# Kernel tuning notes

Hardware: AMD Instinct MI355X
Metric: run time of the kernel (lower is better)

The kernel has to match this reference:

```python
import jax, jax.numpy as jnp
import numpy as np

NUM_ENT = 10000
NUM_REL = 50
HID = 64
N_TRIP = 500000


def _ramp_layer(emb_ent, emb_rel, W_res, W_me, W_mr, W_pr, h, r, t):
    num_ent, num_rel = emb_ent.shape[0], emb_rel.shape[0]
    d_out = W_me.shape[0] // num_rel
    # relation-specific projections: (num_ent, num_rel, d_out), (num_rel, num_rel, d_out)
    proj_ent = (emb_ent @ W_me.T).reshape(num_ent, num_rel, d_out)
    proj_rel = (emb_rel @ W_mr.T).reshape(num_rel, num_rel, d_out)
    diag_rel = proj_rel[jnp.arange(num_rel), jnp.arange(num_rel)]  # (num_rel, d_out)
    # gather per-triplet messages: proj_ent[h, r] + proj_rel[r, r]
    msg = proj_ent[h, r] + diag_rel[r]  # (T, d_out)
    # aggr_method == 'sum' -> div_coeff = 1
    upd = (emb_ent @ W_res.T).at[t].add(msg)  # scatter-add into tails
    return jax.nn.leaky_relu(upd, negative_slope=0.01), emb_rel @ W_pr.T


def setup_inputs() -> dict:
    key = jax.random.key(0)
    ks = jax.random.split(key, 11)
    gain = float(np.sqrt(2.0))  # relu gain

    def xavier(k, shape):
        fan_out, fan_in = shape
        std = gain * np.sqrt(2.0 / (fan_in + fan_out))
        return (jax.random.normal(k, shape, dtype=jnp.float32) * std)

    def msg_init(k, shape, d_in, d_out):
        std = gain * np.sqrt(2.0 / (d_in + d_out))
        return (jax.random.normal(k, shape, dtype=jnp.float32) * std)

    inp = {
        # layer 0: dim_in_ent=NUM_ENT, dim_in_rel=NUM_REL, dim_out=HID
        "Wres0": xavier(ks[0], (HID, NUM_ENT)),
        "Wme0": msg_init(ks[1], (NUM_REL * HID, NUM_ENT), NUM_ENT, HID),
        "Wmr0": msg_init(ks[2], (NUM_REL * HID, NUM_REL), NUM_REL, HID),
        "Wpr0": xavier(ks[3], (HID, NUM_REL)),
        # layer 1: dim_in_ent=HID, dim_in_rel=HID
        "Wres1": xavier(ks[4], (HID, HID)),
        "Wme1": msg_init(ks[5], (NUM_REL * HID, HID), HID, HID),
        "Wmr1": msg_init(ks[6], (NUM_REL * HID, HID), HID, HID),
        "Wpr1": xavier(ks[7], (HID, HID)),
        "h": jax.random.randint(ks[8], (N_TRIP,), 0, NUM_ENT),
        "r": jax.random.randint(ks[9], (N_TRIP,), 0, NUM_REL),
        "t": jax.random.randint(ks[10], (N_TRIP,), 0, NUM_ENT),
    }
    return inp


def reference(Wres0, Wme0, Wmr0, Wpr0, Wres1, Wme1, Wmr1, Wpr1, h, r, t):
    emb_ent = jnp.eye(NUM_ENT, dtype=jnp.float32)
    emb_rel = jnp.eye(NUM_REL, dtype=jnp.float32)
    emb_ent, emb_rel = _ramp_layer(emb_ent, emb_rel, Wres0, Wme0, Wmr0, Wpr0, h, r, t)
    emb_ent, emb_rel = _ramp_layer(emb_ent, emb_rel, Wres1, Wme1, Wmr1, Wpr1, h, r, t)
    return (emb_ent, emb_rel)
```

## Files before the change

### kernel.cpp

```cpp
#include <hip/hip_runtime.h>

#define NUM_ENT 10000
#define NUM_REL 50
#define HID 64
#define NTRIP 500000
#define NSLOT 51
#define SSTR (NUM_ENT * HID)
#define ETILE 128
#define NETILE 79
#define TRB (NSLOT * NETILE)
#define BSTR 192

typedef __attribute__((ext_vector_type(8))) short short8;
typedef __attribute__((ext_vector_type(4))) float f32x4;

static __device__ __forceinline__ unsigned short f2bf(float x) {
    unsigned u = __float_as_uint(x);
    return (unsigned short)((u + 0x7FFFu + ((u >> 16) & 1u)) >> 16);
}
static __device__ __forceinline__ float bf2f(unsigned short b) {
    return __uint_as_float((unsigned)b << 16);
}
static __device__ __forceinline__ short8 ld8(const unsigned short* p) {
    return *(const short8*)p;
}


__global__ __launch_bounds__(256) void k_prep(const float* __restrict__ Wmr0,
                                              const float* __restrict__ Wpr0,
                                              const float* __restrict__ Wmr1,
                                              const float* __restrict__ Wpr1,
                                              const float* __restrict__ Wme1,
                                              const float* __restrict__ Wres1,
                                              int* __restrict__ bins,
                                              float* __restrict__ diag0,
                                              float* __restrict__ diag1,
                                              float* __restrict__ outrel,
                                              unsigned short* __restrict__ Wb) {
    int bid = blockIdx.x, tid = threadIdx.x;
    if (bid < 40) {
        int i = bid * 256 + tid;
        if (i < NUM_ENT) bins[i] = 0;
        return;
    }
    bid -= 40;
    if (bid < 13) {
        int i = bid * 256 + tid;
        if (i < NSLOT * HID)
            diag0[i] = (i < NUM_REL * HID) ? Wmr0[(size_t)i * NUM_REL + (i >> 6)] : 0.f;
        return;
    }
    bid -= 13;
    if (bid < 13) {
        __shared__ float wp[4][64];
        int sub = tid >> 6, d = tid & 63;
        int rr = bid * 4 + sub;
        wp[sub][d] = (rr < NUM_REL) ? Wpr0[d * NUM_REL + rr] : 0.f;
        __syncthreads();
        if (rr < NUM_REL) {
            float s1 = 0.f, s2 = 0.f;
            const float* wmr = Wmr1 + (size_t)(rr * HID + d) * HID;
            const float* wpr = Wpr1 + d * HID;
            for (int k = 0; k < HID; k++) {
                s1 += wp[sub][k] * wmr[k];
                s2 += wp[sub][k] * wpr[k];
            }
            diag1[rr * HID + d] = s1;
            outrel[rr * HID + d] = s2;
        }
        return;
    }
    bid -= 13;
    if (bid < 816) {
        int i = bid * 256 + tid;
        if (i < NSLOT * HID * HID)
            Wb[i] = f2bf(i < NUM_REL * HID * HID ? Wme1[i]
                                                 : Wres1[i - NUM_REL * HID * HID]);
        return;
    }
    if (tid < HID) diag1[NUM_REL * HID + tid] = 0.f;
}


__global__ __launch_bounds__(256) void k_build(const float* __restrict__ Wme0,
                                               const float* __restrict__ Wres0,
                                               const float* __restrict__ diag0,
                                               unsigned short* __restrict__ P,
                                               const int* __restrict__ h,
                                               const int* __restrict__ r,
                                               const int* __restrict__ t,
                                               int* __restrict__ bins,
                                               unsigned* __restrict__ bucket2) {
    __shared__ __align__(16) unsigned utile[ETILE][32];
    __shared__ float dg[64];
    int tid = threadIdx.x;

    if (blockIdx.x >= TRB) {
        int i = ((int)blockIdx.x - TRB) * 256 + tid;
        if (i < NTRIP) {
            int tt = t[i];
            int lp = atomicAdd(&bins[tt], 1);
            if (lp < BSTR)
                bucket2[tt * BSTR + lp] =
                    (unsigned)r[i] * (unsigned)SSTR + (unsigned)h[i] * 64u;
        }
        return;
    }

    int slot = blockIdx.x / NETILE;
    int ey = blockIdx.x - slot * NETILE;
    int e0 = ey * ETILE;
    const float* Wbase = (slot < NUM_REL)
        ? Wme0 + (size_t)(slot * HID) * NUM_ENT + e0
        : Wres0 + e0;
    unsigned short* Pslot = P + (size_t)slot * SSTR;

    if (e0 + ETILE <= NUM_ENT) {
        int dp = tid >> 5;
        int kk = tid & 31;
        int x4 = kk * 4;
        int wf1 = kk & 7;
        int wf2 = kk >> 3;
        const float* p0 = Wbase + (size_t)(dp * 2 + 0) * NUM_ENT + x4;
        const float* p1 = Wbase + (size_t)(dp * 2 + 1) * NUM_ENT + x4;
        float4 vA0 = *(const float4*)(p0);
        float4 vB0 = *(const float4*)(p1);
        float4 vA1 = *(const float4*)(p0 + 16 * NUM_ENT);
        float4 vB1 = *(const float4*)(p1 + 16 * NUM_ENT);
        float4 vA2 = *(const float4*)(p0 + 32 * NUM_ENT);
        float4 vB2 = *(const float4*)(p1 + 32 * NUM_ENT);
        float4 vA3 = *(const float4*)(p0 + 48 * NUM_ENT);
        float4 vB3 = *(const float4*)(p1 + 48 * NUM_ENT);

        if (tid < 64) dg[tid] = diag0[slot * HID + tid];
        __syncthreads();

#define PACK_IT(IT, VA, VB)                                                     \
        {                                                                       \
            int d = IT * 16 + dp * 2;                                           \
            int d2 = IT * 8 + dp;                                               \
            float dgA = dg[d], dgB = dg[d + 1];                                 \
            const float* a = (const float*)&VA;                                 \
            const float* b = (const float*)&VB;                                 \
            int col = (((d2 >> 2) ^ wf1) << 2) | ((d2 & 3) ^ wf2);              \
            utile[x4 + 0][col] = (unsigned)f2bf(a[0] + dgA) |                   \
                                 ((unsigned)f2bf(b[0] + dgB) << 16);            \
            utile[x4 + 1][col] = (unsigned)f2bf(a[1] + dgA) |                   \
                                 ((unsigned)f2bf(b[1] + dgB) << 16);            \
            utile[x4 + 2][col] = (unsigned)f2bf(a[2] + dgA) |                   \
                                 ((unsigned)f2bf(b[2] + dgB) << 16);            \
            utile[x4 + 3][col] = (unsigned)f2bf(a[3] + dgA) |                   \
                                 ((unsigned)f2bf(b[3] + dgB) << 16);            \
        }
        PACK_IT(0, vA0, vB0)
        PACK_IT(1, vA1, vB1)
        PACK_IT(2, vA2, vB2)
        PACK_IT(3, vA3, vB3)
#undef PACK_IT
        __syncthreads();
#pragma unroll
        for (int it = 0; it < 4; ++it) {
            int idx = tid + it * 256;
            int ee = idx >> 3;
            int q = idx & 7;
            int f1 = (ee >> 2) & 7;
            int f2 = (ee >> 5) & 3;
            uint4 u = *(const uint4*)&utile[ee][(q ^ f1) << 2];
            unsigned ua = u.x, ub = u.y, uc = u.z, ud = u.w;
            if (f2 & 1) { unsigned s0 = ua; ua = ub; ub = s0;
                          unsigned s1 = uc; uc = ud; ud = s1; }
            if (f2 & 2) { unsigned s0 = ua; ua = uc; uc = s0;
                          unsigned s1 = ub; ub = ud; ud = s1; }
            uint4 o = make_uint4(ua, ub, uc, ud);
            *(uint4*)&Pslot[(size_t)(e0 + ee) * 64 + q * 8] = o;
        }
    } else {
        if (tid < 64) dg[tid] = diag0[slot * HID + tid];
        __syncthreads();
        int rem = NUM_ENT - e0;
        for (int i = tid; i < rem * 64; i += 256) {
            int ee = i % rem;
            int dd = i / rem;
            float v = Wbase[(size_t)dd * NUM_ENT + ee] + dg[dd];
            Pslot[(size_t)(e0 + ee) * 64 + dd] = f2bf(v);
        }
    }
}


__global__ __launch_bounds__(256) void k_gemmB(const unsigned short* __restrict__ Abf,
                                               const unsigned short* __restrict__ Wb,
                                               const float* __restrict__ diag1,
                                               unsigned short* __restrict__ B,
                                               int percut) {
    int e0 = blockIdx.x * 64;
    int rl0 = blockIdx.y * percut;
    int rl1 = rl0 + percut;
    if (rl1 > NSLOT) rl1 = NSLOT;
    int w = (int)threadIdx.x >> 6;
    int lane = (int)threadIdx.x & 63;
    int lrow = lane & 15;
    int hi = lane >> 4;
    int lk8 = hi * 8;
    int row = e0 + w * 16 + lrow;
    int rowc = row < NUM_ENT ? row : NUM_ENT - 1;
    short8 a0 = ld8(Abf + (size_t)rowc * HID + lk8);
    short8 a1 = ld8(Abf + (size_t)rowc * HID + 32 + lk8);

    for (int rl = rl0; rl < rl1; ++rl) {
        const unsigned short* wb = Wb + (size_t)rl * 4096;
        f32x4 acc[4] = {};
#pragma unroll
        for (int tt = 0; tt < 4; ++tt) {
            const unsigned short* wd = wb + (tt * 16 + lrow) * 64;
            short8 b0 = ld8(wd + lk8);
            short8 b1 = ld8(wd + 32 + lk8);
            acc[tt] = __builtin_amdgcn_mfma_f32_16x16x32_bf16(a0, b0, acc[tt], 0, 0, 0);
            acc[tt] = __builtin_amdgcn_mfma_f32_16x16x32_bf16(a1, b1, acc[tt], 0, 0, 0);
        }
        unsigned short* Bslot = B + (size_t)rl * SSTR;
#pragma unroll
        for (int tt = 0; tt < 4; ++tt) {
            float dgv = diag1[rl * HID + tt * 16 + lrow];
#pragma unroll
            for (int q = 0; q < 4; ++q) {
                int eo = e0 + w * 16 + hi * 4 + q;
                if (eo < NUM_ENT)
                    Bslot[(size_t)eo * 64 + tt * 16 + lrow] = f2bf(acc[tt][q] + dgv);
            }
        }
    }
}


__global__ __launch_bounds__(256) void k_scatter(const unsigned short* __restrict__ table,
                                                 const int* __restrict__ bins,
                                                 const unsigned* __restrict__ bucket2,
                                                 unsigned short* __restrict__ Abf,
                                                 float* __restrict__ outF,
                                                 int writeBf) {
    int e = __builtin_amdgcn_readfirstlane(blockIdx.x * 4 + (threadIdx.x >> 6));
    if (e >= NUM_ENT) return;
    int lane = threadIdx.x & 63;
    int oct = lane >> 3;
    int sl = lane & 7;
    int cnt = bins[e];
    if (cnt > BSTR) cnt = BSTR;
    int j0 = e * BSTR, j1 = j0 + cnt;
    float acc[8] = {};
    float acc2[8] = {};
    int jj = j0;
    for (; jj + 16 <= j1; jj += 16) {
        unsigned o0 = bucket2[jj + oct];
        unsigned o1 = bucket2[jj + 8 + oct];
        short8 v0 = ld8(table + o0 + sl * 8);
        short8 v1 = ld8(table + o1 + sl * 8);
#pragma unroll
        for (int k = 0; k < 8; ++k) {
            acc[k]  += bf2f(((const unsigned short*)&v0)[k]);
            acc2[k] += bf2f(((const unsigned short*)&v1)[k]);
        }
    }
    if (jj + 8 <= j1) {
        unsigned o = bucket2[jj + oct];
        short8 v = ld8(table + o + sl * 8);
#pragma unroll
        for (int k = 0; k < 8; ++k) acc[k] += bf2f(((const unsigned short*)&v)[k]);
        jj += 8;
    }
    if (oct < j1 - jj) {
        unsigned o = bucket2[jj + oct];
        short8 v = ld8(table + o + sl * 8);
#pragma unroll
        for (int k = 0; k < 8; ++k) acc2[k] += bf2f(((const unsigned short*)&v)[k]);
    }
#pragma unroll
    for (int k = 0; k < 8; ++k) {
        acc[k] += acc2[k];
        acc[k] += __shfl_xor(acc[k], 8);
        acc[k] += __shfl_xor(acc[k], 16);
        acc[k] += __shfl_xor(acc[k], 32);
    }
    if (oct == 0) {
        short8 base = ld8(table + (size_t)(NSLOT - 1) * SSTR + (size_t)e * HID + sl * 8);
        float v[8];
#pragma unroll
        for (int k = 0; k < 8; ++k) {
            float x = acc[k] + bf2f(((const unsigned short*)&base)[k]);
            v[k] = (x >= 0.f) ? x : 0.01f * x;
        }
        if (writeBf) {
            unsigned short pk[8];
#pragma unroll
            for (int k = 0; k < 8; ++k) pk[k] = f2bf(v[k]);
            *(short8*)&Abf[(size_t)e * HID + sl * 8] = *(const short8*)pk;
        } else {
            *(float4*)&outF[(size_t)e * HID + sl * 8] = make_float4(v[0], v[1], v[2], v[3]);
            *(float4*)&outF[(size_t)e * HID + sl * 8 + 4] = make_float4(v[4], v[5], v[6], v[7]);
        }
    }
}


__global__ void k_rel(const float* __restrict__ Wpr0, const float* __restrict__ Wmr1,
                      const float* __restrict__ Wpr1, float* __restrict__ diag1,
                      float* __restrict__ outrel) {
    __shared__ float wp[HID];
    int rr = blockIdx.x, d = threadIdx.x;
    wp[d] = Wpr0[d * NUM_REL + rr];
    __syncthreads();
    float s1 = 0.0f, s2 = 0.0f;
    const float* wmr = Wmr1 + (size_t)(rr * HID + d) * HID;
    const float* wpr = Wpr1 + d * HID;
    for (int k = 0; k < HID; k++) { s1 += wp[k] * wmr[k]; s2 += wp[k] * wpr[k]; }
    diag1[rr * HID + d] = s1;
    outrel[rr * HID + d] = s2;
}

__global__ void k_init_u0(const float* __restrict__ Wres0, float* __restrict__ U0) {
    __shared__ float tile[64][65];
    int e0 = blockIdx.x * 64;
    for (int i = threadIdx.x; i < 64 * 64; i += 256) {
        int dd = i >> 6, xx = i & 63;
        if (e0 + xx < NUM_ENT) tile[xx][dd] = Wres0[dd * NUM_ENT + e0 + xx];
    }
    __syncthreads();
    for (int i = threadIdx.x; i < 64 * 64; i += 256) {
        int ee = i >> 6, dd = i & 63;
        if (e0 + ee < NUM_ENT) U0[(e0 + ee) * HID + dd] = tile[ee][dd];
    }
}

__global__ void k_hist(const int* __restrict__ r, int* __restrict__ hist) {
    __shared__ int lh[NUM_REL];
    int tid = threadIdx.x;
    if (tid < NUM_REL) lh[tid] = 0;
    __syncthreads();
    int i = blockIdx.x * blockDim.x + tid;
    if (i < NTRIP) atomicAdd(&lh[r[i]], 1);
    __syncthreads();
    if (tid < NUM_REL && lh[tid] > 0) atomicAdd(&hist[tid], lh[tid]);
}

__global__ void k_scan_small(const int* __restrict__ hist, int* __restrict__ off,
                             int* __restrict__ cur) {
    if (threadIdx.x == 0 && blockIdx.x == 0) {
        int s = 0;
        for (int i = 0; i < NUM_REL; i++) { off[i] = s; cur[i] = s; s += hist[i]; }
        off[NUM_REL] = s;
    }
}

__global__ void k_bucket(const int* __restrict__ h, const int* __restrict__ r,
                         const int* __restrict__ t, int* __restrict__ cur,
                         int2* __restrict__ bucket) {
    __shared__ int lcnt[NUM_REL];
    __shared__ int lbase[NUM_REL];
    int tid = threadIdx.x;
    if (tid < NUM_REL) lcnt[tid] = 0;
    __syncthreads();
    int i = blockIdx.x * blockDim.x + tid;
    int rr = -1, lpos = 0;
    if (i < NTRIP) { rr = r[i]; lpos = atomicAdd(&lcnt[rr], 1); }
    __syncthreads();
    if (tid < NUM_REL && lcnt[tid] > 0) lbase[tid] = atomicAdd(&cur[tid], lcnt[tid]);
    __syncthreads();
    if (i < NTRIP) bucket[lbase[rr] + lpos] = make_int2(h[i], t[i]);
}

__global__ void k_l0(const float* __restrict__ Wme0, const float* __restrict__ Wmr0,
                     const int* __restrict__ off, const int2* __restrict__ bucket,
                     float* __restrict__ U0) {
    __shared__ float row[NUM_ENT];
    int rr = blockIdx.x >> 6;
    int d  = blockIdx.x & 63;
    const float4* src4 = (const float4*)(Wme0 + (size_t)(rr * HID + d) * NUM_ENT);
    float4* row4 = (float4*)row;
    for (int i = threadIdx.x; i < NUM_ENT / 4; i += blockDim.x) row4[i] = src4[i];
    __syncthreads();
    float wd0 = Wmr0[(size_t)(rr * HID + d) * NUM_REL + rr];
    int b0 = off[rr], b1 = off[rr + 1];
    for (int i = b0 + threadIdx.x; i < b1; i += blockDim.x) {
        int2 ht = bucket[i];
        atomicAdd(&U0[(size_t)ht.y * HID + d], row[ht.x] + wd0);
    }
}

__global__ void k_lrelu(float* __restrict__ x, int n) {
    int i = blockIdx.x * blockDim.x + threadIdx.x;
    if (i < n) { float v = x[i]; x[i] = v >= 0.0f ? v : 0.01f * v; }
}

__global__ void k_init_u1(const float* __restrict__ A, const float* __restrict__ Wres1,
                          float* __restrict__ out) {
    __shared__ float W[HID][HID + 1];
    int tid = threadIdx.x;
    for (int i = tid; i < HID * HID; i += 256) W[i >> 6][i & 63] = Wres1[i];
    __syncthreads();
    int g = blockIdx.x * 256 + tid;
    int e = g >> 6, d = g & 63;
    if (e >= NUM_ENT) return;
    const float4* arow = (const float4*)(A + (size_t)e * HID);
    float acc = 0.0f;
#pragma unroll
    for (int k4 = 0; k4 < 16; k4++) {
        float4 a = arow[k4];
        acc = fmaf(a.x, W[d][k4 * 4 + 0], acc);
        acc = fmaf(a.y, W[d][k4 * 4 + 1], acc);
        acc = fmaf(a.z, W[d][k4 * 4 + 2], acc);
        acc = fmaf(a.w, W[d][k4 * 4 + 3], acc);
    }
    out[g] = acc;
}

#define L1_CHUNKS 16
__global__ void k_l1(const float* __restrict__ A, const float* __restrict__ Wme1,
                     const int* __restrict__ off, const int2* __restrict__ bucket,
                     const float* __restrict__ diag1, float* __restrict__ out) {
    int rr = blockIdx.x / L1_CHUNKS;
    int chunk = blockIdx.x % L1_CHUNKS;
    int b0 = off[rr], b1 = off[rr + 1];
    for (int i = b0 + chunk * 256 + (int)threadIdx.x; i < b1; i += L1_CHUNKS * 256) {
        int2 ht = bucket[i];
        const float4* arow = (const float4*)(A + (size_t)ht.x * HID);
        float4 a[16];
#pragma unroll
        for (int j = 0; j < 16; j++) a[j] = arow[j];
        float* op = out + (size_t)ht.y * HID;
#pragma unroll 4
        for (int d = 0; d < HID; d++) {
            const float4* m4 = (const float4*)(Wme1 + (size_t)(rr * HID + d) * HID);
            float acc = diag1[rr * HID + d];
#pragma unroll
            for (int k = 0; k < 16; k++) {
                float4 m = m4[k];
                acc = fmaf(a[k].x, m.x, acc);
                acc = fmaf(a[k].y, m.y, acc);
                acc = fmaf(a[k].z, m.z, acc);
                acc = fmaf(a[k].w, m.w, acc);
            }
            atomicAdd(op + d, acc);
        }
    }
}


static inline size_t align_up(size_t x, size_t a) { return (x + a - 1) & ~(a - 1); }

extern "C" void kernel_launch(void* const* d_in, const int* in_sizes, int n_in,
                              void* d_out, int out_size, void* d_ws, size_t ws_size,
                              hipStream_t stream) {
    const float* Wres0 = (const float*)d_in[0];
    const float* Wme0  = (const float*)d_in[1];
    const float* Wmr0  = (const float*)d_in[2];
    const float* Wpr0  = (const float*)d_in[3];
    const float* Wres1 = (const float*)d_in[4];
    const float* Wme1  = (const float*)d_in[5];
    const float* Wmr1  = (const float*)d_in[6];
    const float* Wpr1  = (const float*)d_in[7];
    const int* h = (const int*)d_in[8];
    const int* r = (const int*)d_in[9];
    const int* t = (const int*)d_in[10];
    float* out = (float*)d_out;

    char* ws = (char*)d_ws;
    const int nbt = (NTRIP + 255) / 256;
    const int net = (NUM_ENT + 63) / 64;

    size_t p = 0;
    size_t oTab  = p; p += align_up((size_t)NSLOT * SSTR * 2, 256);
    size_t oB2   = p; p += align_up((size_t)NUM_ENT * BSTR * 4, 256);
    size_t oBins = p; p += align_up((size_t)NUM_ENT * 4, 256);
    size_t oAbf  = p; p += align_up((size_t)NUM_ENT * HID * 2, 256);
    size_t oD0   = p; p += align_up((size_t)NSLOT * HID * 4, 256);
    size_t oD1   = p; p += align_up((size_t)NSLOT * HID * 4, 256);
    size_t oWb   = p; p += align_up((size_t)NSLOT * HID * HID * 2, 256);
    size_t need = p;

    if (need <= ws_size) {
        unsigned short* Tab = (unsigned short*)(ws + oTab);
        unsigned* bucket2   = (unsigned*)(ws + oB2);
        int*      bins      = (int*)(ws + oBins);
        unsigned short* Abf = (unsigned short*)(ws + oAbf);
        float*    diag0     = (float*)(ws + oD0);
        float*    diag1     = (float*)(ws + oD1);
        unsigned short* Wb  = (unsigned short*)(ws + oWb);
        const int nsplit = 6;
        const int percut = (NSLOT + nsplit - 1) / nsplit;

        k_prep<<<883, 256, 0, stream>>>(Wmr0, Wpr0, Wmr1, Wpr1, Wme1, Wres1,
                                        bins, diag0, diag1, out + NUM_ENT * HID, Wb);
        k_build<<<TRB + nbt, 256, 0, stream>>>(Wme0, Wres0, diag0, Tab,
                                               h, r, t, bins, bucket2);
        k_scatter<<<(NUM_ENT + 3) / 4, 256, 0, stream>>>(
            Tab, bins, bucket2, Abf, out, 1);
        k_gemmB<<<dim3(net, nsplit), 256, 0, stream>>>(Abf, Wb, diag1, Tab, percut);
        k_scatter<<<(NUM_ENT + 3) / 4, 256, 0, stream>>>(
            Tab, bins, bucket2, Abf, out, 0);
        return;
    }

    {
        int2*  bucket = (int2*)ws;
        float* U0     = (float*)(ws + 4000000);
        float* diag1  = (float*)(ws + 6560000);
        int*   hist   = (int*)(ws + 6572800);
        int*   off    = (int*)(ws + 6573056);
        int*   cur    = (int*)(ws + 6573312);

        hipMemsetAsync(hist, 0, NUM_REL * sizeof(int), stream);
        k_hist<<<nbt, 256, 0, stream>>>(r, hist);
        k_scan_small<<<1, 64, 0, stream>>>(hist, off, cur);
        k_bucket<<<nbt, 256, 0, stream>>>(h, r, t, cur, bucket);

        k_init_u0<<<net, 256, 0, stream>>>(Wres0, U0);
        k_l0<<<NUM_REL * HID, 256, 0, stream>>>(Wme0, Wmr0, off, bucket, U0);
        k_lrelu<<<(NUM_ENT * HID + 255) / 256, 256, 0, stream>>>(U0, NUM_ENT * HID);

        k_rel<<<NUM_REL, HID, 0, stream>>>(Wpr0, Wmr1, Wpr1, diag1, out + NUM_ENT * HID);
        k_init_u1<<<(NUM_ENT * HID) / 256, 256, 0, stream>>>(U0, Wres1, out);
        k_l1<<<NUM_REL * L1_CHUNKS, 256, 0, stream>>>(U0, Wme1, off, bucket, diag1, out);
        k_lrelu<<<(NUM_ENT * HID + 255) / 256, 256, 0, stream>>>(out, NUM_ENT * HID);
    }
}
```

Measured before the change: 150.9 us.

## Store layer-0 gather table in FP8 and widen gemmB tiles to 256 rows

The layer-0 projection table is now quantized to a custom e4m3-style FP8 encoding instead of bf16, which halves the bytes written by the build kernel and read by the first scatter gather. The scatter kernel is templated to decode FP8 or bf16. Separately, the layer-1 gemm now has each wave compute four 16-row tiles that reuse the same B fragments, and the relation split is raised to 13. The FP8 quantization loses precision in the layer-0 messages, which risks exceeding the accuracy tolerance, and the software encode/decode adds ALU work.

```diff
diff --git a/kernel.cpp b/kernel.cpp
--- a/kernel.cpp
+++ b/kernel.cpp
@@ -23,6 +23,32 @@
 }
 static __device__ __forceinline__ short8 ld8(const unsigned short* p) {
     return *(const short8*)p;
+}
+
+static __device__ __forceinline__ unsigned f2fp8(float x) {
+    unsigned u = __float_as_uint(x);
+    unsigned s = (u >> 24) & 0x80u;
+    float a = __uint_as_float(u & 0x7fffffffu);
+    unsigned code;
+    if (a >= 0.015625f) {
+        unsigned r = (u & 0x7fffffffu) + 0x7FFFFu + ((u >> 20) & 1u);
+        int e = (int)((r >> 23) & 0xff) - 127;
+        unsigned m = (r >> 20) & 7u;
+        if (e > 8) { e = 8; m = 6; }
+        if (e == 8 && m == 7) m = 6;
+        code = ((unsigned)(e + 7) << 3) | m;
+    } else {
+        code = (unsigned)__float2int_rn(a * 512.0f);
+    }
+    return code | s;
+}
+static __device__ __forceinline__ float fp8dec(unsigned c) {
+    unsigned e = (c >> 3) & 15u;
+    unsigned m = c & 7u;
+    unsigned mm = m + (e ? 8u : 0u);
+    unsigned eb = (e ? e : 1u) + 117u;
+    float f = (float)mm * __uint_as_float(eb << 23);
+    return (c & 0x80u) ? -f : f;
 }
 
 
@@ -85,7 +111,7 @@
 __global__ __launch_bounds__(256) void k_build(const float* __restrict__ Wme0,
                                                const float* __restrict__ Wres0,
                                                const float* __restrict__ diag0,
-                                               unsigned short* __restrict__ P,
+                                               unsigned char* __restrict__ P8,
                                                const int* __restrict__ h,
                                                const int* __restrict__ r,
                                                const int* __restrict__ t,
@@ -113,7 +139,7 @@
     const float* Wbase = (slot < NUM_REL)
         ? Wme0 + (size_t)(slot * HID) * NUM_ENT + e0
         : Wres0 + e0;
-    unsigned short* Pslot = P + (size_t)slot * SSTR;
+    unsigned char* Pslot = P8 + (size_t)slot * SSTR;
 
     if (e0 + ETILE <= NUM_ENT) {
         int dp = tid >> 5;
@@ -171,8 +197,15 @@
                           unsigned s1 = uc; uc = ud; ud = s1; }
             if (f2 & 2) { unsigned s0 = ua; ua = uc; uc = s0;
                           unsigned s1 = ub; ub = ud; ud = s1; }
-            uint4 o = make_uint4(ua, ub, uc, ud);
-            *(uint4*)&Pslot[(size_t)(e0 + ee) * 64 + q * 8] = o;
+            unsigned lo = f2fp8(bf2f((unsigned short)ua))
+                        | (f2fp8(bf2f((unsigned short)(ua >> 16))) << 8)
+                        | (f2fp8(bf2f((unsigned short)ub)) << 16)
+                        | (f2fp8(bf2f((unsigned short)(ub >> 16))) << 24);
+            unsigned hi = f2fp8(bf2f((unsigned short)uc))
+                        | (f2fp8(bf2f((unsigned short)(uc >> 16))) << 8)
+                        | (f2fp8(bf2f((unsigned short)ud)) << 16)
+                        | (f2fp8(bf2f((unsigned short)(ud >> 16))) << 24);
+            *(uint2*)&Pslot[(size_t)(e0 + ee) * 64 + q * 8] = make_uint2(lo, hi);
         }
     } else {
         if (tid < 64) dg[tid] = diag0[slot * HID + tid];
@@ -182,7 +215,7 @@
             int ee = i % rem;
             int dd = i / rem;
             float v = Wbase[(size_t)dd * NUM_ENT + ee] + dg[dd];
-            Pslot[(size_t)(e0 + ee) * 64 + dd] = f2bf(v);
+            Pslot[(size_t)(e0 + ee) * 64 + dd] = (unsigned char)f2fp8(v);
         }
     }
 }
@@ -193,7 +226,7 @@
                                                const float* __restrict__ diag1,
                                                unsigned short* __restrict__ B,
                                                int percut) {
-    int e0 = blockIdx.x * 64;
+    int e0 = blockIdx.x * 256;
     int rl0 = blockIdx.y * percut;
     int rl1 = rl0 + percut;
     if (rl1 > NSLOT) rl1 = NSLOT;
@@ -202,38 +235,52 @@
     int lrow = lane & 15;
     int hi = lane >> 4;
     int lk8 = hi * 8;
-    int row = e0 + w * 16 + lrow;
-    int rowc = row < NUM_ENT ? row : NUM_ENT - 1;
-    short8 a0 = ld8(Abf + (size_t)rowc * HID + lk8);
-    short8 a1 = ld8(Abf + (size_t)rowc * HID + 32 + lk8);
+    int ew = e0 + w * 64;
+
+    short8 am0[4], am1[4];
+#pragma unroll
+    for (int m = 0; m < 4; ++m) {
+        int row = ew + m * 16 + lrow;
+        int rowc = row < NUM_ENT ? row : NUM_ENT - 1;
+        am0[m] = ld8(Abf + (size_t)rowc * HID + lk8);
+        am1[m] = ld8(Abf + (size_t)rowc * HID + 32 + lk8);
+    }
 
     for (int rl = rl0; rl < rl1; ++rl) {
         const unsigned short* wb = Wb + (size_t)rl * 4096;
-        f32x4 acc[4] = {};
+        f32x4 acc[4][4] = {};
 #pragma unroll
         for (int tt = 0; tt < 4; ++tt) {
             const unsigned short* wd = wb + (tt * 16 + lrow) * 64;
             short8 b0 = ld8(wd + lk8);
             short8 b1 = ld8(wd + 32 + lk8);
-            acc[tt] = __builtin_amdgcn_mfma_f32_16x16x32_bf16(a0, b0, acc[tt], 0, 0, 0);
-            acc[tt] = __builtin_amdgcn_mfma_f32_16x16x32_bf16(a1, b1, acc[tt], 0, 0, 0);
+#pragma unroll
+            for (int m = 0; m < 4; ++m) {
+                acc[m][tt] = __builtin_amdgcn_mfma_f32_16x16x32_bf16(am0[m], b0, acc[m][tt], 0, 0, 0);
+                acc[m][tt] = __builtin_amdgcn_mfma_f32_16x16x32_bf16(am1[m], b1, acc[m][tt], 0, 0, 0);
+            }
         }
         unsigned short* Bslot = B + (size_t)rl * SSTR;
 #pragma unroll
-        for (int tt = 0; tt < 4; ++tt) {
-            float dgv = diag1[rl * HID + tt * 16 + lrow];
-#pragma unroll
-            for (int q = 0; q < 4; ++q) {
-                int eo = e0 + w * 16 + hi * 4 + q;
-                if (eo < NUM_ENT)
-                    Bslot[(size_t)eo * 64 + tt * 16 + lrow] = f2bf(acc[tt][q] + dgv);
+        for (int m = 0; m < 4; ++m) {
+#pragma unroll
+            for (int tt = 0; tt < 4; ++tt) {
+                float dgv = diag1[rl * HID + tt * 16 + lrow];
+#pragma unroll
+                for (int q = 0; q < 4; ++q) {
+                    int eo = ew + m * 16 + hi * 4 + q;
+                    if (eo < NUM_ENT)
+                        Bslot[(size_t)eo * 64 + tt * 16 + lrow] =
+                            f2bf(acc[m][tt][q] + dgv);
+                }
             }
         }
     }
 }
 
 
-__global__ __launch_bounds__(256) void k_scatter(const unsigned short* __restrict__ table,
+template <int FP8>
+__global__ __launch_bounds__(256) void k_scatter(const unsigned char* __restrict__ table,
                                                  const int* __restrict__ bins,
                                                  const unsigned* __restrict__ bucket2,
                                                  unsigned short* __restrict__ Abf,
@@ -250,30 +297,36 @@
     float acc[8] = {};
     float acc2[8] = {};
     int jj = j0;
+#define GATHER8(O, ACC)                                                          \
+    {                                                                            \
+        if (FP8) {                                                               \
+            uint2 v = *(const uint2*)(table + (size_t)(O) + sl * 8);             \
+            ACC[0] += fp8dec(v.x & 255); ACC[1] += fp8dec((v.x >> 8) & 255);     \
+            ACC[2] += fp8dec((v.x >> 16) & 255); ACC[3] += fp8dec(v.x >> 24);    \
+            ACC[4] += fp8dec(v.y & 255); ACC[5] += fp8dec((v.y >> 8) & 255);     \
+            ACC[6] += fp8dec((v.y >> 16) & 255); ACC[7] += fp8dec(v.y >> 24);    \
+        } else {                                                                 \
+            short8 v = ld8((const unsigned short*)(table + 2 * (size_t)(O)) + sl * 8); \
+            for (int k = 0; k < 8; ++k)                                          \
+                ACC[k] += bf2f(((const unsigned short*)&v)[k]);                  \
+        }                                                                        \
+    }
     for (; jj + 16 <= j1; jj += 16) {
         unsigned o0 = bucket2[jj + oct];
         unsigned o1 = bucket2[jj + 8 + oct];
-        short8 v0 = ld8(table + o0 + sl * 8);
-        short8 v1 = ld8(table + o1 + sl * 8);
-#pragma unroll
-        for (int k = 0; k < 8; ++k) {
-            acc[k]  += bf2f(((const unsigned short*)&v0)[k]);
-            acc2[k] += bf2f(((const unsigned short*)&v1)[k]);
-        }
+        GATHER8(o0, acc)
+        GATHER8(o1, acc2)
     }
     if (jj + 8 <= j1) {
         unsigned o = bucket2[jj + oct];
-        short8 v = ld8(table + o + sl * 8);
-#pragma unroll
-        for (int k = 0; k < 8; ++k) acc[k] += bf2f(((const unsigned short*)&v)[k]);
+        GATHER8(o, acc)
         jj += 8;
     }
     if (oct < j1 - jj) {
         unsigned o = bucket2[jj + oct];
-        short8 v = ld8(table + o + sl * 8);
-#pragma unroll
-        for (int k = 0; k < 8; ++k) acc2[k] += bf2f(((const unsigned short*)&v)[k]);
-    }
+        GATHER8(o, acc2)
+    }
+#undef GATHER8
 #pragma unroll
     for (int k = 0; k < 8; ++k) {
         acc[k] += acc2[k];
@@ -282,11 +335,23 @@
         acc[k] += __shfl_xor(acc[k], 32);
     }
     if (oct == 0) {
-        short8 base = ld8(table + (size_t)(NSLOT - 1) * SSTR + (size_t)e * HID + sl * 8);
+        size_t baseo = (size_t)(NSLOT - 1) * SSTR + (size_t)e * HID;
+        float bse[8];
+        if (FP8) {
+            uint2 v = *(const uint2*)(table + baseo + sl * 8);
+            bse[0] = fp8dec(v.x & 255); bse[1] = fp8dec((v.x >> 8) & 255);
+            bse[2] = fp8dec((v.x >> 16) & 255); bse[3] = fp8dec(v.x >> 24);
+            bse[4] = fp8dec(v.y & 255); bse[5] = fp8dec((v.y >> 8) & 255);
+            bse[6] = fp8dec((v.y >> 16) & 255); bse[7] = fp8dec(v.y >> 24);
+        } else {
+            short8 v = ld8((const unsigned short*)(table + 2 * baseo) + sl * 8);
+#pragma unroll
+            for (int k = 0; k < 8; ++k) bse[k] = bf2f(((const unsigned short*)&v)[k]);
+        }
         float v[8];
 #pragma unroll
         for (int k = 0; k < 8; ++k) {
-            float x = acc[k] + bf2f(((const unsigned short*)&base)[k]);
+            float x = acc[k] + bse[k];
             v[k] = (x >= 0.f) ? x : 0.01f * x;
         }
         if (writeBf) {
@@ -465,7 +530,6 @@
 
     char* ws = (char*)d_ws;
     const int nbt = (NTRIP + 255) / 256;
-    const int net = (NUM_ENT + 63) / 64;
 
     size_t p = 0;
     size_t oTab  = p; p += align_up((size_t)NSLOT * SSTR * 2, 256);
@@ -478,29 +542,33 @@
     size_t need = p;
 
     if (need <= ws_size) {
-        unsigned short* Tab = (unsigned short*)(ws + oTab);
+        unsigned char*  Tab8 = (unsigned char*)(ws + oTab);
+        unsigned short* TabH = (unsigned short*)(ws + oTab);
         unsigned* bucket2   = (unsigned*)(ws + oB2);
         int*      bins      = (int*)(ws + oBins);
         unsigned short* Abf = (unsigned short*)(ws + oAbf);
         float*    diag0     = (float*)(ws + oD0);
         float*    diag1     = (float*)(ws + oD1);
         unsigned short* Wb  = (unsigned short*)(ws + oWb);
-        const int nsplit = 6;
+        const int netile256 = (NUM_ENT + 255) / 256;
+        const int nsplit = 13;
         const int percut = (NSLOT + nsplit - 1) / nsplit;
 
         k_prep<<<883, 256, 0, stream>>>(Wmr0, Wpr0, Wmr1, Wpr1, Wme1, Wres1,
                                         bins, diag0, diag1, out + NUM_ENT * HID, Wb);
-        k_build<<<TRB + nbt, 256, 0, stream>>>(Wme0, Wres0, diag0, Tab,
+        k_build<<<TRB + nbt, 256, 0, stream>>>(Wme0, Wres0, diag0, Tab8,
                                                h, r, t, bins, bucket2);
-        k_scatter<<<(NUM_ENT + 3) / 4, 256, 0, stream>>>(
-            Tab, bins, bucket2, Abf, out, 1);
-        k_gemmB<<<dim3(net, nsplit), 256, 0, stream>>>(Abf, Wb, diag1, Tab, percut);
-        k_scatter<<<(NUM_ENT + 3) / 4, 256, 0, stream>>>(
-            Tab, bins, bucket2, Abf, out, 0);
+        k_scatter<1><<<(NUM_ENT + 3) / 4, 256, 0, stream>>>(
+            Tab8, bins, bucket2, Abf, out, 1);
+        k_gemmB<<<dim3(netile256, nsplit), 256, 0, stream>>>(Abf, Wb, diag1, TabH,
+                                                             percut);
+        k_scatter<0><<<(NUM_ENT + 3) / 4, 256, 0, stream>>>(
+            Tab8, bins, bucket2, Abf, out, 0);
         return;
     }
 
     {
+        const int net = (NUM_ENT + 63) / 64;
         int2*  bucket = (int2*)ws;
         float* U0     = (float*)(ws + 4000000);
         float* diag1  = (float*)(ws + 6560000);
```

Result: faster. 136.3 us, median of 2 (-9.7%).
